# Performance work log

Hardware: AMD Instinct MI355X
Metric: run time of the kernel (lower is better)

Reference implementation:

```python
import jax, jax.numpy as jnp
import numpy as np
import math

EMBED_DIM = 1024
NUM_HEADS = 16
HEAD_DIM = EMBED_DIM // NUM_HEADS
WINDOW_SIZE = 32  # one-sided; full window = 2*w+1 = 65
SCALING = math.sqrt(HEAD_DIM)


def setup_inputs() -> dict:
    key = jax.random.key(0)
    ks = jax.random.split(key, 9)
    B, S, E = 2, 2048, EMBED_DIM
    s = 1.0 / math.sqrt(E)
    inp = {
        "hidden_states": jax.random.normal(ks[0], (B, S, E), dtype=jnp.float32),
        "q_w": jax.random.uniform(ks[1], (E, E), jnp.float32, -s, s),
        "q_b": jax.random.uniform(ks[2], (E,), jnp.float32, -s, s),
        "k_w": jax.random.uniform(ks[3], (E, E), jnp.float32, -s, s),
        "k_b": jax.random.uniform(ks[4], (E,), jnp.float32, -s, s),
        "v_w": jax.random.uniform(ks[5], (E, E), jnp.float32, -s, s),
        "v_b": jax.random.uniform(ks[6], (E,), jnp.float32, -s, s),
        "o_w": jax.random.uniform(ks[7], (E, E), jnp.float32, -s, s),
        "o_b": jax.random.uniform(ks[8], (E,), jnp.float32, -s, s),
    }
    return inp


def reference(hidden_states, q_w, q_b, k_w, k_b, v_w, v_b, o_w, o_b):
    B, S, E = hidden_states.shape
    H, D, w = NUM_HEADS, HEAD_DIM, WINDOW_SIZE
    W = 2 * w + 1

    q = hidden_states @ q_w.T + q_b
    k = hidden_states @ k_w.T + k_b
    v = hidden_states @ v_w.T + v_b

    # [B, H, S, D]
    q = q.reshape(B, S, H, D).transpose(0, 2, 1, 3)
    k = k.reshape(B, S, H, D).transpose(0, 2, 1, 3)
    v = v.reshape(B, S, H, D).transpose(0, 2, 1, 3)

    # zero-pad seq dim by w on each side (matches F.pad value=0); padded keys
    # contribute score 0 (NOT -inf) exactly like the original unfold scheme.
    k_pad = jnp.pad(k, ((0, 0), (0, 0), (w, w), (0, 0)))
    v_pad = jnp.pad(v, ((0, 0), (0, 0), (w, w), (0, 0)))

    # window gather indices: query i sees padded positions i..i+2w (orig i-w..i+w)
    idx = jnp.arange(S)[:, None] + jnp.arange(W)[None, :]  # [S, W]
    k_slice = k_pad[:, :, idx]  # [B, H, S, W, D]
    v_slice = v_pad[:, :, idx]  # [B, H, S, W, D]

    score = jnp.einsum('bhsd,bhswd->bhsw', q, k_slice) / SCALING
    p = jax.nn.softmax(score, axis=-1)
    attn = jnp.einsum('bhsw,bhswd->bhsd', p, v_slice)

    attn = attn.transpose(0, 2, 1, 3).reshape(B, S, E)
    return attn @ o_w.T + o_b
```

## Files before the change

kernel.cpp:

```cpp
#include <hip/hip_runtime.h>
#include <math.h>

typedef _Float16 h16;
typedef _Float16 h8 __attribute__((ext_vector_type(8)));
typedef float f32x4 __attribute__((ext_vector_type(4)));

__device__ inline void gl2lds16(const void* g, void* l) {
  __builtin_amdgcn_global_load_lds(
      (const __attribute__((address_space(1))) void*)g,
      (__attribute__((address_space(3))) void*)l, 16, 0, 0);
}

__device__ inline void barrier_raw() {
  asm volatile("" ::: "memory");
  __builtin_amdgcn_s_barrier();
  asm volatile("" ::: "memory");
}

#define VMCNT(N) asm volatile("s_waitcnt vmcnt(" #N ")" ::: "memory")
#define LGKM(N) asm volatile("s_waitcnt lgkmcnt(" #N ")" ::: "memory")

__global__ __launch_bounds__(256) void f2h_all(
    const float* __restrict__ hs, const float* __restrict__ w0,
    const float* __restrict__ w1, const float* __restrict__ w2,
    const float* __restrict__ w3, h16* __restrict__ dst, int hsN) {
  int i = (blockIdx.x * 256 + threadIdx.x) * 8;
  const int tot = hsN + 4 * 1048576;
  if (i >= tot) return;
  const float* src;
  int off;
  if (i < hsN) {
    src = hs; off = i;
  } else {
    int k = i - hsN;
    int seg = k >> 20;
    off = k & 1048575;
    src = seg == 0 ? w0 : seg == 1 ? w1 : seg == 2 ? w2 : w3;
  }
  float4 a = *(const float4*)(src + off);
  float4 b = *(const float4*)(src + off + 4);
  h8 o;
  o[0] = (h16)a.x; o[1] = (h16)a.y; o[2] = (h16)a.z; o[3] = (h16)a.w;
  o[4] = (h16)b.x; o[5] = (h16)b.y; o[6] = (h16)b.z; o[7] = (h16)b.w;
  *(h8*)(dst + i) = o;
}

__global__ __launch_bounds__(512, 2) void qkv8(
    const h16* __restrict__ A, const h16* __restrict__ Bw,
    const float* __restrict__ qb, const float* __restrict__ kb,
    const float* __restrict__ vb, h16* __restrict__ qo, h16* __restrict__ ko,
    h16* __restrict__ vo, int nbm, int cpx) {
  __shared__ __align__(16) h16 Asm[2][256][64];
  __shared__ __align__(16) h16 Bsm[2][256][64];

  const int tid = threadIdx.x;
  const int wid = tid >> 6, lane = tid & 63;
  const int lr = lane & 15, lg = lane >> 4;
  const int wr = wid >> 2, wc = wid & 3;
  const int srow = wid * 8 + (lane >> 3);
  const int lsrc = ((lane & 7) ^ (srow & 7)) * 8;

  const int wg = (blockIdx.x % 8) * cpx + blockIdx.x / 8;
  const int bm = wg % nbm, bn = wg / nbm;
  const int row0 = bm * 256, col0 = bn * 256;

  const h16* Ag = A + (size_t)row0 * 1024;
  const h16* Bg = Bw + (size_t)col0 * 1024;

  auto stg = [&](const h16* g, h16* l, int rs) {
    gl2lds16(g + (size_t)(rs + srow) * 1024 + lsrc, l + (rs + wid * 8) * 64);
  };
  auto ldf = [&](const h16* base, int row, int kk) -> h8 {
    return *(const h8*)(base + row * 64 + ((kk * 4 + lg) ^ (lr & 7)) * 8);
  };

  f32x4 acc[8][4] = {};
  h8 bf[4][2], afA[2][2], afB[2][2];

  stg(Ag, &Asm[0][0][0], 0);   stg(Ag, &Asm[0][0][0], 128);
  stg(Bg, &Bsm[0][0][0], 0);   stg(Bg, &Bsm[0][0][0], 64);
  stg(Bg, &Bsm[0][0][0], 128); stg(Bg, &Bsm[0][0][0], 192);
  stg(Ag, &Asm[0][0][0], 64);  stg(Ag, &Asm[0][0][0], 192);
  VMCNT(2);
  barrier_raw();

#define MMA2(AF, M0)                                                           \
  __builtin_amdgcn_s_setprio(1);                                               \
  _Pragma("unroll") for (int kk = 0; kk < 2; ++kk)                             \
      _Pragma("unroll") for (int mi = 0; mi < 2; ++mi)                         \
          _Pragma("unroll") for (int n = 0; n < 4; ++n)                        \
              acc[(M0) + mi][n] = __builtin_amdgcn_mfma_f32_16x16x32_f16(      \
                  AF[mi][kk], bf[n][kk], acc[(M0) + mi][n], 0, 0, 0);          \
  __builtin_amdgcn_s_setprio(0)

#define TILE_PHASES(T, RBUF, WBUF)                                             \
  {                                                                            \
    const h16* Ar = &Asm[RBUF][0][0];                                          \
    const h16* Br = &Bsm[RBUF][0][0];                                          \
    h16* Aw = &Asm[WBUF][0][0];                                                \
    h16* Bwl = &Bsm[WBUF][0][0];                                               \
    const h16* Agt = Ag + (size_t)((T) + 1) * 64;                              \
    const h16* Bgt = Bg + (size_t)((T) + 1) * 64;                              \
    const bool st = (T) < 15;                                                  \
    _Pragma("unroll") for (int n = 0; n < 4; ++n) {                            \
      bf[n][0] = ldf(Br, wc * 64 + n * 16 + lr, 0);                            \
      bf[n][1] = ldf(Br, wc * 64 + n * 16 + lr, 1);                            \
    }                                                                          \
    _Pragma("unroll") for (int kk = 0; kk < 2; ++kk) {                         \
      afA[0][kk] = ldf(Ar, wr * 128 + 0 * 16 + lr, kk);                        \
      afA[1][kk] = ldf(Ar, wr * 128 + 1 * 16 + lr, kk);                        \
    }                                                                          \
    _Pragma("unroll") for (int kk = 0; kk < 2; ++kk) {                         \
      afB[0][kk] = ldf(Ar, wr * 128 + 2 * 16 + lr, kk);                        \
      afB[1][kk] = ldf(Ar, wr * 128 + 3 * 16 + lr, kk);                        \
    }                                                                          \
    if (st) { stg(Agt, Aw, 0); stg(Agt, Aw, 128); }                            \
    barrier_raw();                                                             \
    LGKM(4);                                                                   \
    MMA2(afA, 0);                                                              \
    if (st) { VMCNT(2); } else { VMCNT(0); }                                   \
    barrier_raw();                                                             \
    _Pragma("unroll") for (int kk = 0; kk < 2; ++kk) {                         \
      afA[0][kk] = ldf(Ar, wr * 128 + 4 * 16 + lr, kk);                        \
      afA[1][kk] = ldf(Ar, wr * 128 + 5 * 16 + lr, kk);                        \
    }                                                                          \
    if (st) { stg(Bgt, Bwl, 0); stg(Bgt, Bwl, 64); }                           \
    barrier_raw();                                                             \
    LGKM(4);                                                                   \
    MMA2(afB, 2);                                                              \
    barrier_raw();                                                             \
    _Pragma("unroll") for (int kk = 0; kk < 2; ++kk) {                         \
      afB[0][kk] = ldf(Ar, wr * 128 + 6 * 16 + lr, kk);                        \
      afB[1][kk] = ldf(Ar, wr * 128 + 7 * 16 + lr, kk);                        \
    }                                                                          \
    if (st) { stg(Bgt, Bwl, 128); stg(Bgt, Bwl, 192); }                        \
    barrier_raw();                                                             \
    LGKM(4);                                                                   \
    MMA2(afA, 4);                                                              \
    barrier_raw();                                                             \
    if (st) { stg(Agt, Aw, 64); stg(Agt, Aw, 192); }                           \
    barrier_raw();                                                             \
    LGKM(0);                                                                   \
    MMA2(afB, 6);                                                              \
    if (st) { VMCNT(2); } else { VMCNT(0); }                                   \
    barrier_raw();                                                             \
  }

  for (int tt = 0; tt < 16; tt += 2) {
    TILE_PHASES(tt, 0, 1);
    TILE_PHASES(tt + 1, 1, 0);
  }
#undef TILE_PHASES
#undef MMA2

  const int tsel = col0 >> 10;
  const float* bp = tsel == 0 ? qb : (tsel == 1 ? kb : vb);
  h16* outp = tsel == 0 ? qo : (tsel == 1 ? ko : vo);
#pragma unroll
  for (int n = 0; n < 4; ++n) {
    const int cidx = col0 + wc * 64 + n * 16 + lr;
    const int jj = cidx & 1023;
    const float bv = bp[jj];
    const int hh = jj >> 6, dd = jj & 63;
#pragma unroll
    for (int m = 0; m < 8; ++m) {
#pragma unroll
      for (int j = 0; j < 4; ++j) {
        const int r = row0 + wr * 128 + m * 16 + lg * 4 + j;
        const int bb = r >> 11, ss = r & 2047;
        outp[(((size_t)bb * 16 + hh) * 2048 + ss) * 64 + dd] =
            (h16)(acc[m][n][j] + bv);
      }
    }
  }
}

__global__ __launch_bounds__(64) void oproj1w(const h16* __restrict__ A,
                                              const h16* __restrict__ Bw,
                                              const float* __restrict__ b0,
                                              float* __restrict__ Cf) {
  __shared__ __align__(16) h16 Ash[2][32][64];
  __shared__ __align__(16) h16 Bsh[2][128][64];

  const int lane = threadIdx.x;
  const int lr = lane & 15, lg = lane >> 4;
  const int srw = lane >> 3;
  const int csw = ((lane & 7) ^ (srw & 7)) * 8;

  const int wg = (blockIdx.x & 7) * 128 + (blockIdx.x >> 3);
  const int bm = wg & 127, bn = wg >> 7;
  const int row0 = bm * 32, col0 = bn * 128;

  const h16* Ag = A + (size_t)row0 * 1024;
  const h16* Bg = Bw + (size_t)col0 * 1024;

  auto stage = [&](int t, int bi) {
    const int kof = t * 64 + csw;
#pragma unroll
    for (int rs = 0; rs < 32; rs += 8)
      gl2lds16(Ag + (size_t)(rs + srw) * 1024 + kof, &Ash[bi][rs][0]);
#pragma unroll
    for (int rs = 0; rs < 128; rs += 8)
      gl2lds16(Bg + (size_t)(rs + srw) * 1024 + kof, &Bsh[bi][rs][0]);
  };
  auto ldf = [&](const h16* base, int row, int kk) -> h8 {
    return *(const h8*)(base + row * 64 + ((kk * 4 + lg) ^ (row & 7)) * 8);
  };

  f32x4 acc[2][8] = {};

  stage(0, 0);
  for (int t = 0; t < 16; ++t) {
    if (t + 1 < 16) {
      stage(t + 1, (t + 1) & 1);
      VMCNT(20);
    } else {
      VMCNT(0);
    }
    const h16* Ar = &Ash[t & 1][0][0];
    const h16* Br = &Bsh[t & 1][0][0];
    h8 af[2][2], bf[8][2];
#pragma unroll
    for (int m = 0; m < 2; ++m)
#pragma unroll
      for (int kk = 0; kk < 2; ++kk) af[m][kk] = ldf(Ar, m * 16 + lr, kk);
#pragma unroll
    for (int n = 0; n < 8; ++n)
#pragma unroll
      for (int kk = 0; kk < 2; ++kk) bf[n][kk] = ldf(Br, n * 16 + lr, kk);
    __builtin_amdgcn_s_setprio(1);
#pragma unroll
    for (int m = 0; m < 2; ++m)
#pragma unroll
      for (int n = 0; n < 8; ++n)
#pragma unroll
        for (int kk = 0; kk < 2; ++kk)
          acc[m][n] = __builtin_amdgcn_mfma_f32_16x16x32_f16(af[m][kk], bf[n][kk],
                                                             acc[m][n], 0, 0, 0);
    __builtin_amdgcn_s_setprio(0);
  }

#pragma unroll
  for (int n = 0; n < 8; ++n) {
    const int cidx = col0 + n * 16 + lr;
    const float bv = b0[cidx];
#pragma unroll
    for (int m = 0; m < 2; ++m)
#pragma unroll
      for (int j = 0; j < 4; ++j) {
        const int r = row0 + m * 16 + lg * 4 + j;
        Cf[(size_t)r * 1024 + cidx] = acc[m][n][j] + bv;
      }
  }
}

__global__ __launch_bounds__(256) void swattn(const h16* __restrict__ Q,
                                              const h16* __restrict__ K,
                                              const h16* __restrict__ V,
                                              h16* __restrict__ O) {
  __shared__ __align__(16) h16 Ksh[128 * 72];
  __shared__ __align__(16) h16 Vsh[64 * 136];
  __shared__ __align__(16) h16 Psh[4][16 * 136];

  const int qb0 = blockIdx.x * 64;
  const int bh = blockIdx.y;
  const int b = bh >> 4, h = bh & 15;
  const int tid = threadIdx.x;
  const int wave = tid >> 6, lane = tid & 63;
  const int lr = lane & 15, lg = lane >> 4;

  const h16* Qb = Q + (size_t)bh * 2048 * 64;
  const h16* Kb = K + (size_t)bh * 2048 * 64;
  const h16* Vb = V + (size_t)bh * 2048 * 64;

#pragma unroll
  for (int i = 0; i < 4; ++i) {
    const int c = tid * 4 + i;
    const int row = c >> 3, c8 = c & 7;
    const int t = qb0 - 32 + row;
    h8 kv, vv;
    if (t >= 0 && t < 2048) {
      kv = *(const h8*)&Kb[(size_t)t * 64 + c8 * 8];
      vv = *(const h8*)&Vb[(size_t)t * 64 + c8 * 8];
    } else {
#pragma unroll
      for (int j = 0; j < 8; ++j) { kv[j] = (h16)0.f; vv[j] = (h16)0.f; }
    }
    *(h8*)&Ksh[row * 72 + c8 * 8] = kv;
#pragma unroll
    for (int j = 0; j < 8; ++j) Vsh[(c8 * 8 + j) * 136 + row] = vv[j];
  }
  __syncthreads();

  const int qrow = qb0 + wave * 16 + lr;
  h8 qa[2];
#pragma unroll
  for (int kk = 0; kk < 2; ++kk)
    qa[kk] = *(const h8*)&Qb[(size_t)qrow * 64 + kk * 32 + lg * 8];

  f32x4 sacc[8] = {};
#pragma unroll
  for (int n = 0; n < 8; ++n)
#pragma unroll
    for (int kk = 0; kk < 2; ++kk) {
      h8 kb = *(const h8*)&Ksh[(n * 16 + lr) * 72 + kk * 32 + lg * 8];
      sacc[n] = __builtin_amdgcn_mfma_f32_16x16x32_f16(qa[kk], kb, sacc[n], 0, 0, 0);
    }

  float p[8][4];
#pragma unroll
  for (int j = 0; j < 4; ++j) {
    const int wrow = wave * 16 + lg * 4 + j;
    float mx = -1e30f;
#pragma unroll
    for (int n = 0; n < 8; ++n) {
      const int d = n * 16 + lr - wrow;
      float s = (d < 0 || d > 64) ? -1e30f : sacc[n][j] * 0.125f;
      p[n][j] = s;
      mx = fmaxf(mx, s);
    }
#pragma unroll
    for (int off = 1; off < 16; off <<= 1) mx = fmaxf(mx, __shfl_xor(mx, off, 64));
    float sum = 0.f;
#pragma unroll
    for (int n = 0; n < 8; ++n) {
      const float e = __expf(p[n][j] - mx);
      p[n][j] = e;
      sum += e;
    }
#pragma unroll
    for (int off = 1; off < 16; off <<= 1) sum += __shfl_xor(sum, off, 64);
    const float inv = 1.f / sum;
#pragma unroll
    for (int n = 0; n < 8; ++n) p[n][j] *= inv;
  }

#pragma unroll
  for (int n = 0; n < 8; ++n)
#pragma unroll
    for (int j = 0; j < 4; ++j)
      Psh[wave][(lg * 4 + j) * 136 + n * 16 + lr] = (h16)p[n][j];
  __syncthreads();

  f32x4 oacc[4] = {};
#pragma unroll
  for (int kk = 0; kk < 4; ++kk) {
    h8 pa = *(const h8*)&Psh[wave][lr * 136 + kk * 32 + lg * 8];
#pragma unroll
    for (int n = 0; n < 4; ++n) {
      h8 vb = *(const h8*)&Vsh[(n * 16 + lr) * 136 + kk * 32 + lg * 8];
      oacc[n] = __builtin_amdgcn_mfma_f32_16x16x32_f16(pa, vb, oacc[n], 0, 0, 0);
    }
  }

#pragma unroll
  for (int n = 0; n < 4; ++n)
#pragma unroll
    for (int j = 0; j < 4; ++j) {
      const int s = qb0 + wave * 16 + lg * 4 + j;
      const int d = n * 16 + lr;
      O[((size_t)b * 2048 + s) * 1024 + h * 64 + d] = (h16)oacc[n][j];
    }
}

extern "C" void kernel_launch(void* const* d_in, const int* in_sizes, int n_in,
                              void* d_out, int out_size, void* d_ws, size_t ws_size,
                              hipStream_t stream) {
  const float* hs = (const float*)d_in[0];
  const float* qw = (const float*)d_in[1];
  const float* qb = (const float*)d_in[2];
  const float* kw = (const float*)d_in[3];
  const float* kb = (const float*)d_in[4];
  const float* vw = (const float*)d_in[5];
  const float* vb = (const float*)d_in[6];
  const float* ow = (const float*)d_in[7];
  const float* ob = (const float*)d_in[8];

  const int M = in_sizes[0] / 1024;

  h16* hsH = (h16*)d_ws;
  h16* wqkv = hsH + (size_t)M * 1024;
  h16* woH = wqkv + (size_t)3072 * 1024;
  h16* qH = woH + (size_t)1024 * 1024;
  h16* kH = qH + (size_t)M * 1024;
  h16* vH = kH + (size_t)M * 1024;
  h16* attnH = vH + (size_t)M * 1024;

  const int tot = M * 1024 + 4 * 1048576;
  f2h_all<<<(tot / 8 + 255) / 256, 256, 0, stream>>>(hs, qw, kw, vw, ow, hsH,
                                                     M * 1024);

  const int nbm = M / 256;
  const int nwg = nbm * 12;
  qkv8<<<nwg, 512, 0, stream>>>(hsH, wqkv, qb, kb, vb, qH, kH, vH, nbm, nwg / 8);

  swattn<<<dim3(32, M / 2048 * 16), 256, 0, stream>>>(qH, kH, vH, attnH);

  oproj1w<<<1024, 64, 0, stream>>>(attnH, woH, ob, (float*)d_out);
}
```

Measured before the change: 86.81 us.

## Replace QKV GEMM with simpler 128x128 tile kernel and row-major Q/K/V output

Swaps the hand-pipelined 256x256-tile, 512-thread, double-buffered QKV GEMM for a simpler 128x128-tile, 256-thread kernel that stages 32-wide K slices with a barrier around each step. The output is staged through LDS and written row-major as [B,S,E] with coalesced 16-byte stores, instead of scattered stores into a [B,H,S,D] layout. The attention kernel is changed to read Q/K/V with a 1024-element row stride to match. This gives more workgroups (768) and coalesced epilogue stores, but loses double buffering and load/compute overlap in the main loop and adds two syncs per K step.

```diff
diff --git a/kernel.cpp b/kernel.cpp
--- a/kernel.cpp
+++ b/kernel.cpp
@@ -11,14 +11,7 @@
       (__attribute__((address_space(3))) void*)l, 16, 0, 0);
 }
 
-__device__ inline void barrier_raw() {
-  asm volatile("" ::: "memory");
-  __builtin_amdgcn_s_barrier();
-  asm volatile("" ::: "memory");
-}
-
 #define VMCNT(N) asm volatile("s_waitcnt vmcnt(" #N ")" ::: "memory")
-#define LGKM(N) asm volatile("s_waitcnt lgkmcnt(" #N ")" ::: "memory")
 
 __global__ __launch_bounds__(256) void f2h_all(
     const float* __restrict__ hs, const float* __restrict__ w0,
@@ -45,133 +38,81 @@
   *(h8*)(dst + i) = o;
 }
 
-__global__ __launch_bounds__(512, 2) void qkv8(
+__global__ __launch_bounds__(256) void qkv97(
     const h16* __restrict__ A, const h16* __restrict__ Bw,
     const float* __restrict__ qb, const float* __restrict__ kb,
     const float* __restrict__ vb, h16* __restrict__ qo, h16* __restrict__ ko,
-    h16* __restrict__ vo, int nbm, int cpx) {
-  __shared__ __align__(16) h16 Asm[2][256][64];
-  __shared__ __align__(16) h16 Bsm[2][256][64];
+    h16* __restrict__ vo) {
+  __shared__ __align__(16) h16 Ash[128 * 32];
+  __shared__ __align__(16) h16 Bsh[128 * 32];
+  __shared__ __align__(16) h16 Csh[128 * 136];
 
   const int tid = threadIdx.x;
   const int wid = tid >> 6, lane = tid & 63;
   const int lr = lane & 15, lg = lane >> 4;
-  const int wr = wid >> 2, wc = wid & 3;
-  const int srow = wid * 8 + (lane >> 3);
-  const int lsrc = ((lane & 7) ^ (srow & 7)) * 8;
-
-  const int wg = (blockIdx.x % 8) * cpx + blockIdx.x / 8;
-  const int bm = wg % nbm, bn = wg / nbm;
-  const int row0 = bm * 256, col0 = bn * 256;
+  const int wr = wid >> 1, wc = wid & 1;
+  const int srow = tid >> 2;
+  const int csw = ((tid & 3) ^ ((srow >> 1) & 3)) * 8;
+
+  const int wg = (blockIdx.x & 7) * 96 + (blockIdx.x >> 3);
+  const int bm = wg & 31, bn = wg >> 5;
+  const int row0 = bm * 128, col0 = bn * 128;
 
   const h16* Ag = A + (size_t)row0 * 1024;
   const h16* Bg = Bw + (size_t)col0 * 1024;
 
-  auto stg = [&](const h16* g, h16* l, int rs) {
-    gl2lds16(g + (size_t)(rs + srow) * 1024 + lsrc, l + (rs + wid * 8) * 64);
+  auto ldf = [&](const h16* base, int row) -> h8 {
+    return *(const h8*)(base + row * 32 + (lg ^ ((row >> 1) & 3)) * 8);
   };
-  auto ldf = [&](const h16* base, int row, int kk) -> h8 {
-    return *(const h8*)(base + row * 64 + ((kk * 4 + lg) ^ (lr & 7)) * 8);
-  };
-
-  f32x4 acc[8][4] = {};
-  h8 bf[4][2], afA[2][2], afB[2][2];
-
-  stg(Ag, &Asm[0][0][0], 0);   stg(Ag, &Asm[0][0][0], 128);
-  stg(Bg, &Bsm[0][0][0], 0);   stg(Bg, &Bsm[0][0][0], 64);
-  stg(Bg, &Bsm[0][0][0], 128); stg(Bg, &Bsm[0][0][0], 192);
-  stg(Ag, &Asm[0][0][0], 64);  stg(Ag, &Asm[0][0][0], 192);
-  VMCNT(2);
-  barrier_raw();
-
-#define MMA2(AF, M0)                                                           \
-  __builtin_amdgcn_s_setprio(1);                                               \
-  _Pragma("unroll") for (int kk = 0; kk < 2; ++kk)                             \
-      _Pragma("unroll") for (int mi = 0; mi < 2; ++mi)                         \
-          _Pragma("unroll") for (int n = 0; n < 4; ++n)                        \
-              acc[(M0) + mi][n] = __builtin_amdgcn_mfma_f32_16x16x32_f16(      \
-                  AF[mi][kk], bf[n][kk], acc[(M0) + mi][n], 0, 0, 0);          \
-  __builtin_amdgcn_s_setprio(0)
-
-#define TILE_PHASES(T, RBUF, WBUF)                                             \
-  {                                                                            \
-    const h16* Ar = &Asm[RBUF][0][0];                                          \
-    const h16* Br = &Bsm[RBUF][0][0];                                          \
-    h16* Aw = &Asm[WBUF][0][0];                                                \
-    h16* Bwl = &Bsm[WBUF][0][0];                                               \
-    const h16* Agt = Ag + (size_t)((T) + 1) * 64;                              \
-    const h16* Bgt = Bg + (size_t)((T) + 1) * 64;                              \
-    const bool st = (T) < 15;                                                  \
-    _Pragma("unroll") for (int n = 0; n < 4; ++n) {                            \
-      bf[n][0] = ldf(Br, wc * 64 + n * 16 + lr, 0);                            \
-      bf[n][1] = ldf(Br, wc * 64 + n * 16 + lr, 1);                            \
-    }                                                                          \
-    _Pragma("unroll") for (int kk = 0; kk < 2; ++kk) {                         \
-      afA[0][kk] = ldf(Ar, wr * 128 + 0 * 16 + lr, kk);                        \
-      afA[1][kk] = ldf(Ar, wr * 128 + 1 * 16 + lr, kk);                        \
-    }                                                                          \
-    _Pragma("unroll") for (int kk = 0; kk < 2; ++kk) {                         \
-      afB[0][kk] = ldf(Ar, wr * 128 + 2 * 16 + lr, kk);                        \
-      afB[1][kk] = ldf(Ar, wr * 128 + 3 * 16 + lr, kk);                        \
-    }                                                                          \
-    if (st) { stg(Agt, Aw, 0); stg(Agt, Aw, 128); }                            \
-    barrier_raw();                                                             \
-    LGKM(4);                                                                   \
-    MMA2(afA, 0);                                                              \
-    if (st) { VMCNT(2); } else { VMCNT(0); }                                   \
-    barrier_raw();                                                             \
-    _Pragma("unroll") for (int kk = 0; kk < 2; ++kk) {                         \
-      afA[0][kk] = ldf(Ar, wr * 128 + 4 * 16 + lr, kk);                        \
-      afA[1][kk] = ldf(Ar, wr * 128 + 5 * 16 + lr, kk);                        \
-    }                                                                          \
-    if (st) { stg(Bgt, Bwl, 0); stg(Bgt, Bwl, 64); }                           \
-    barrier_raw();                                                             \
-    LGKM(4);                                                                   \
-    MMA2(afB, 2);                                                              \
-    barrier_raw();                                                             \
-    _Pragma("unroll") for (int kk = 0; kk < 2; ++kk) {                         \
-      afB[0][kk] = ldf(Ar, wr * 128 + 6 * 16 + lr, kk);                        \
-      afB[1][kk] = ldf(Ar, wr * 128 + 7 * 16 + lr, kk);                        \
-    }                                                                          \
-    if (st) { stg(Bgt, Bwl, 128); stg(Bgt, Bwl, 192); }                        \
-    barrier_raw();                                                             \
-    LGKM(4);                                                                   \
-    MMA2(afA, 4);                                                              \
-    barrier_raw();                                                             \
-    if (st) { stg(Agt, Aw, 64); stg(Agt, Aw, 192); }                           \
-    barrier_raw();                                                             \
-    LGKM(0);                                                                   \
-    MMA2(afB, 6);                                                              \
-    if (st) { VMCNT(2); } else { VMCNT(0); }                                   \
-    barrier_raw();                                                             \
-  }
-
-  for (int tt = 0; tt < 16; tt += 2) {
-    TILE_PHASES(tt, 0, 1);
-    TILE_PHASES(tt + 1, 1, 0);
-  }
-#undef TILE_PHASES
-#undef MMA2
-
-  const int tsel = col0 >> 10;
+
+  f32x4 acc[4][4] = {};
+
+  for (int t = 0; t < 32; ++t) {
+    const int kof = t * 32 + csw;
+    gl2lds16(Ag + (size_t)srow * 1024 + kof, &Ash[(wid * 16) * 32]);
+    gl2lds16(Ag + (size_t)(64 + srow) * 1024 + kof, &Ash[(64 + wid * 16) * 32]);
+    gl2lds16(Bg + (size_t)srow * 1024 + kof, &Bsh[(wid * 16) * 32]);
+    gl2lds16(Bg + (size_t)(64 + srow) * 1024 + kof, &Bsh[(64 + wid * 16) * 32]);
+    __syncthreads();
+    h8 af[4], bf[4];
+#pragma unroll
+    for (int m = 0; m < 4; ++m) af[m] = ldf(Ash, wr * 64 + m * 16 + lr);
+#pragma unroll
+    for (int n = 0; n < 4; ++n) bf[n] = ldf(Bsh, wc * 64 + n * 16 + lr);
+    __builtin_amdgcn_s_setprio(1);
+#pragma unroll
+    for (int m = 0; m < 4; ++m)
+#pragma unroll
+      for (int n = 0; n < 4; ++n)
+        acc[m][n] =
+            __builtin_amdgcn_mfma_f32_16x16x32_f16(af[m], bf[n], acc[m][n], 0, 0, 0);
+    __builtin_amdgcn_s_setprio(0);
+    __syncthreads();
+  }
+
+  const int tsel = bn >> 3;
+  const int colseg = (bn & 7) * 128;
   const float* bp = tsel == 0 ? qb : (tsel == 1 ? kb : vb);
   h16* outp = tsel == 0 ? qo : (tsel == 1 ? ko : vo);
+
 #pragma unroll
   for (int n = 0; n < 4; ++n) {
-    const int cidx = col0 + wc * 64 + n * 16 + lr;
-    const int jj = cidx & 1023;
-    const float bv = bp[jj];
-    const int hh = jj >> 6, dd = jj & 63;
-#pragma unroll
-    for (int m = 0; m < 8; ++m) {
-#pragma unroll
-      for (int j = 0; j < 4; ++j) {
-        const int r = row0 + wr * 128 + m * 16 + lg * 4 + j;
-        const int bb = r >> 11, ss = r & 2047;
-        outp[(((size_t)bb * 16 + hh) * 2048 + ss) * 64 + dd] =
+    const int ccol = wc * 64 + n * 16 + lr;
+    const float bv = bp[colseg + ccol];
+#pragma unroll
+    for (int m = 0; m < 4; ++m)
+#pragma unroll
+      for (int j = 0; j < 4; ++j)
+        Csh[(wr * 64 + m * 16 + lg * 4 + j) * 136 + ccol] =
             (h16)(acc[m][n][j] + bv);
-      }
-    }
+  }
+  __syncthreads();
+#pragma unroll
+  for (int p = 0; p < 8; ++p) {
+    const int idx = p * 256 + tid;
+    const int r = idx >> 4, c = idx & 15;
+    h8 v = *(const h8*)&Csh[r * 136 + c * 8];
+    *(h8*)&outp[(size_t)(row0 + r) * 1024 + colseg + c * 8] = v;
   }
 }
 
@@ -269,9 +210,9 @@
   const int wave = tid >> 6, lane = tid & 63;
   const int lr = lane & 15, lg = lane >> 4;
 
-  const h16* Qb = Q + (size_t)bh * 2048 * 64;
-  const h16* Kb = K + (size_t)bh * 2048 * 64;
-  const h16* Vb = V + (size_t)bh * 2048 * 64;
+  const h16* Qb = Q + (size_t)b * 2048 * 1024 + h * 64;
+  const h16* Kb = K + (size_t)b * 2048 * 1024 + h * 64;
+  const h16* Vb = V + (size_t)b * 2048 * 1024 + h * 64;
 
 #pragma unroll
   for (int i = 0; i < 4; ++i) {
@@ -280,8 +221,8 @@
     const int t = qb0 - 32 + row;
     h8 kv, vv;
     if (t >= 0 && t < 2048) {
-      kv = *(const h8*)&Kb[(size_t)t * 64 + c8 * 8];
-      vv = *(const h8*)&Vb[(size_t)t * 64 + c8 * 8];
+      kv = *(const h8*)&Kb[(size_t)t * 1024 + c8 * 8];
+      vv = *(const h8*)&Vb[(size_t)t * 1024 + c8 * 8];
     } else {
 #pragma unroll
       for (int j = 0; j < 8; ++j) { kv[j] = (h16)0.f; vv[j] = (h16)0.f; }
@@ -296,7 +237,7 @@
   h8 qa[2];
 #pragma unroll
   for (int kk = 0; kk < 2; ++kk)
-    qa[kk] = *(const h8*)&Qb[(size_t)qrow * 64 + kk * 32 + lg * 8];
+    qa[kk] = *(const h8*)&Qb[(size_t)qrow * 1024 + kk * 32 + lg * 8];
 
   f32x4 sacc[8] = {};
 #pragma unroll
@@ -390,9 +331,7 @@
   f2h_all<<<(tot / 8 + 255) / 256, 256, 0, stream>>>(hs, qw, kw, vw, ow, hsH,
                                                      M * 1024);
 
-  const int nbm = M / 256;
-  const int nwg = nbm * 12;
-  qkv8<<<nwg, 512, 0, stream>>>(hsH, wqkv, qb, kb, vb, qH, kH, vH, nbm, nwg / 8);
+  qkv97<<<768, 256, 0, stream>>>(hsH, wqkv, qb, kb, vb, qH, kH, vH);
 
   swattn<<<dim3(32, M / 2048 * 16), 256, 0, stream>>>(qH, kH, vH, attnH);
 
```

Result: no change. 86.65 us (-0.2%).
